# Kernel optimization log

Hardware: AMD Instinct MI355X
Metric: run time of the kernel (lower is better)

Reference implementation:

```python
import jax, jax.numpy as jnp
import numpy as np

DIM = 1024
HEAD_DIM = 64
NUM_HEADS = DIM // HEAD_DIM
SCALE = HEAD_DIM ** -0.5
B, N, M = 2, 1024, 2048


def setup_inputs() -> dict:
    key = jax.random.key(0)
    ks = jax.random.split(key, 7)
    x = jax.random.normal(ks[0], (B, N, DIM), dtype=jnp.float32)
    context = jax.random.normal(ks[1], (B, M, DIM), dtype=jnp.float32)
    # query row has at least one valid key (avoids all -inf softmax rows).
    mask = jax.random.bernoulli(ks[2], 0.9, (B, N, M))
    mask = mask.at[:, :, 0].set(True)
    # Linear params (torch nn.Linear convention: y = x @ W.T + b)
    sq = (1.0 / DIM) ** 0.5
    Wq = jax.random.uniform(ks[3], (DIM, DIM), minval=-sq, maxval=sq, dtype=jnp.float32)
    Wkv = jax.random.uniform(ks[4], (2 * DIM, DIM), minval=-sq, maxval=sq, dtype=jnp.float32)
    b_kv = jax.random.uniform(ks[5], (2 * DIM,), minval=-sq, maxval=sq, dtype=jnp.float32)
    Wo = jax.random.uniform(ks[6], (DIM, DIM), minval=-sq, maxval=sq, dtype=jnp.float32)
    return {"x": x, "context": context, "mask": mask,
            "Wq": Wq, "Wkv": Wkv, "b_kv": b_kv, "Wo": Wo}


def reference(x, context, mask, Wq, Wkv, b_kv, Wo):
    b, n, c = x.shape
    m = context.shape[1]
    h, d = NUM_HEADS, HEAD_DIM
    # Q projection (no bias): [b, n, h, d] -> bhnd
    q = (x @ Wq.T).reshape(b, n, h, d).transpose(0, 2, 1, 3)
    # KV projection (with bias): [b, m, 2, h, d]
    kv = (context @ Wkv.T + b_kv).reshape(b, m, 2, h, d)
    k = kv[:, :, 0].transpose(0, 2, 1, 3)  # bhmd
    v = kv[:, :, 1].transpose(0, 2, 1, 3)  # bhmd
    # scores: bhnm, scale applied after matmul as in the original
    attn = jnp.einsum('bhnd,bhmd->bhnm', q, k) * SCALE
    attn = jnp.where(mask[:, None, :, :], attn, -jnp.inf)
    attn = jax.nn.softmax(attn, axis=-1)
    out = jnp.einsum('bhnm,bhmd->bhnd', attn, v)
    out = out.transpose(0, 2, 1, 3).reshape(b, n, h * d)
    return out @ Wo.T
```

## Files before the change

kernel.cpp:

```cpp
#include <hip/hip_runtime.h>


typedef __attribute__((ext_vector_type(8))) short short8;
typedef __attribute__((ext_vector_type(4))) short short4v;
typedef __attribute__((ext_vector_type(4))) float f32x4;

#define SCL2E 0.18033688011112042592f

__device__ __forceinline__ float bf2f(short s) {
  unsigned u = ((unsigned)(unsigned short)s) << 16;
  return __uint_as_float(u);
}
__device__ __forceinline__ short f2bf(float f) {
  unsigned u = __float_as_uint(f);
  u += 0x7fffu + ((u >> 16) & 1u);
  return (short)(u >> 16);
}
__device__ __forceinline__ void gld_lds16(const void* gp, void* lp) {
  __builtin_amdgcn_global_load_lds(
      (const __attribute__((address_space(1))) unsigned int*)gp,
      (__attribute__((address_space(3))) unsigned int*)lp, 16, 0, 0);
}
__device__ __forceinline__ short4v cvt4(float4 v) {
  short4v o;
  o[0] = f2bf(v.x); o[1] = f2bf(v.y); o[2] = f2bf(v.z); o[3] = f2bf(v.w);
  return o;
}

__global__ __launch_bounds__(256) void prep(
    const unsigned char* __restrict__ mask, unsigned long long* __restrict__ pm,
    const float* __restrict__ Wq, const float* __restrict__ Wkv,
    const float* __restrict__ Wo, const float* __restrict__ x,
    const float* __restrict__ ctx, short* __restrict__ wqb,
    short* __restrict__ wkvb, short* __restrict__ wob,
    short* __restrict__ xb, short* __restrict__ ctxb) {
  const int row = blockIdx.x;
  const int wave = threadIdx.x >> 6, lane = threadIdx.x & 63;
  const unsigned char p8 = mask[lane * 4 + 1];
  const int p32 = ((const int*)mask)[lane * 2 + 1];
  const int shift =
      (__ballot(p8 != 0) != 0ull) ? 0 : ((__ballot(p32 != 0) != 0ull) ? 2 : 3);
  const size_t base = ((size_t)row * 2048) << shift;
#pragma unroll
  for (int j = 0; j < 8; j++) {
    const int c = wave * 512 + j * 64 + lane;
    const unsigned long long bits = __ballot(mask[base + ((size_t)c << shift)] != 0);
    if (lane == 0) pm[(size_t)row * 32 + wave * 8 + j] = bits;
  }
  const int gid = blockIdx.x * 256 + threadIdx.x;
  *(short4v*)(xb + (size_t)gid * 4) = cvt4(((const float4*)x)[gid]);
  *(short4v*)(ctxb + (size_t)gid * 4) = cvt4(((const float4*)ctx)[gid]);
  *(short4v*)(ctxb + (size_t)(gid + 524288) * 4) =
      cvt4(((const float4*)ctx)[gid + 524288]);
  *(short4v*)(wkvb + (size_t)gid * 4) = cvt4(((const float4*)Wkv)[gid]);
  if (gid < 262144) {
    *(short4v*)(wqb + (size_t)gid * 4) = cvt4(((const float4*)Wq)[gid]);
    *(short4v*)(wob + (size_t)gid * 4) = cvt4(((const float4*)Wo)[gid]);
  }
}

__global__ __launch_bounds__(256, 2)
void qkv_gemm(const short* __restrict__ xb, const short* __restrict__ ctxb,
              const short* __restrict__ wqb, const short* __restrict__ wkvb,
              const float* __restrict__ bias, short* __restrict__ qws,
              short* __restrict__ kws, short* __restrict__ vtws) {
  __shared__ __align__(16) short ldsA[8 * 512];
  __shared__ __align__(16) short ldsB[8 * 512];
  const int tid = threadIdx.x;
  const int wave = tid >> 6, lane = tid & 63;
  const int l15 = lane & 15, lg = lane >> 4;
  const int bx = blockIdx.x;
  const bool isKV = bx < 512;
  const int rows0 = isKV ? (bx >> 4) * 128 : ((bx - 512) >> 3) * 128;
  const int cols0 = isKV ? (bx & 15) * 128 : ((bx - 512) & 7) * 128;
  const short* Amat = isKV ? ctxb : xb;
  const short* Bw = isKV ? wkvb : wqb;
  const int wr = wave >> 1, wc = wave & 1;

  f32x4 acc[4][4];
#pragma unroll
  for (int i = 0; i < 4; i++)
#pragma unroll
    for (int j = 0; j < 4; j++) acc[i][j] = (f32x4){0.f, 0.f, 0.f, 0.f};

  const short* ga0 = Amat + (size_t)(rows0 + wave * 16 + l15) * 1024 + lg * 8;
  const short* ga1 = ga0 + (size_t)64 * 1024;
  const short* gb0 = Bw + (size_t)(cols0 + wave * 16 + l15) * 1024 + lg * 8;
  const short* gb1 = gb0 + (size_t)64 * 1024;
  short* la0 = &ldsA[wave * 512];
  short* la1 = &ldsA[(wave + 4) * 512];
  short* lb0 = &ldsB[wave * 512];
  short* lb1 = &ldsB[(wave + 4) * 512];

  for (int k0 = 0; k0 < 1024; k0 += 32) {
    __syncthreads();
    gld_lds16(ga0 + k0, la0);
    gld_lds16(ga1 + k0, la1);
    gld_lds16(gb0 + k0, lb0);
    gld_lds16(gb1 + k0, lb1);
    __syncthreads();
    short8 af[4], bfr[4];
#pragma unroll
    for (int t = 0; t < 4; t++)
      af[t] = *(const short8*)&ldsA[((wr * 4 + t) * 64 + lane) * 8];
#pragma unroll
    for (int t = 0; t < 4; t++)
      bfr[t] = *(const short8*)&ldsB[((wc * 4 + t) * 64 + lane) * 8];
#pragma unroll
    for (int i = 0; i < 4; i++)
#pragma unroll
      for (int j = 0; j < 4; j++)
        acc[i][j] =
            __builtin_amdgcn_mfma_f32_16x16x32_bf16(af[i], bfr[j], acc[i][j], 0, 0, 0);
  }

#pragma unroll
  for (int i = 0; i < 4; i++)
#pragma unroll
    for (int j = 0; j < 4; j++)
#pragma unroll
      for (int r = 0; r < 4; r++) {
        const int gr = rows0 + wr * 64 + i * 16 + lg * 4 + r;
        const int gc = cols0 + wc * 64 + j * 16 + l15;
        float v = acc[i][j][r];
        if (isKV) {
          v += bias[gc];
          const int b = gr >> 11, m = gr & 2047;
          const int kv = gc >> 10, hh = (gc >> 6) & 15, d = gc & 63;
          if (kv == 0)
            kws[((((size_t)b * 16 + hh) * 2048 + m) << 6) + d] = f2bf(v);
          else
            vtws[(((size_t)b * 16 + hh) * 64 + d) * 2048 + m] = f2bf(v);
        } else {
          const int b = gr >> 10, n = gr & 1023, hh = gc >> 6, d = gc & 63;
          qws[((((size_t)b * 16 + hh) * 1024 + n) << 6) + d] = f2bf(v * SCL2E);
        }
      }
}

__global__ __launch_bounds__(512, 2)
void attn_split(const short* __restrict__ Qg, const short* __restrict__ Kg,
                const short* __restrict__ Vtg,
                const unsigned int* __restrict__ pm,
                float* __restrict__ opart, float* __restrict__ lpart) {
  __shared__ __align__(16) short ldsK[8192];
  __shared__ __align__(16) short ldsV[8192];
  __shared__ __align__(16) short ldsP[17408];
  __shared__ __align__(16) short ones[512];
  const int tid = threadIdx.x;
  const int w = tid >> 6, lane = tid & 63;
  const int l15 = lane & 15, lg = lane >> 4;
  const int bx = blockIdx.x;
  const int bhid = bx & 31, qt = (bx >> 5) & 7, half = bx >> 8;
  const int b = bhid >> 4, h = bhid & 15;
  const int n0 = qt * 128, m_base = half * 1024;
  const size_t bh = (size_t)b * 16 + h;
  const short* Qb = Qg + (bh * 1024 + n0) * 64;
  const short* Kb = Kg + (bh << 17);
  const short* Vb = Vtg + (bh << 17);
  const unsigned int* pmw =
      pm + ((size_t)(b * 1024 + n0 + w * 16 + lg * 4) << 6) + (m_base >> 5);

  ones[tid] = 0x3F80;
#pragma unroll
  for (int ii = 0; ii < 2; ii++)
    gld_lds16(Qb + (size_t)(w * 16 + l15) * 64 + ii * 32 + lg * 8,
              &ldsP[(w * 2 + ii) * 512]);
  __syncthreads();
  short8 qf[2];
#pragma unroll
  for (int ks = 0; ks < 2; ks++)
    qf[ks] = *(const short8*)&ldsP[((w * 2 + ks) * 64 + lane) * 8];
  const short8 onesf = *(const short8*)&ones[lane * 8];

  f32x4 o[4], lacc;
#pragma unroll
  for (int ct = 0; ct < 4; ct++) o[ct] = (f32x4){0.f, 0.f, 0.f, 0.f};
  lacc = (f32x4){0.f, 0.f, 0.f, 0.f};
  short* Pme = &ldsP[w * 2176];

  uint4 mk[4], mkn[4];
#pragma unroll
  for (int r = 0; r < 4; r++) mk[r] = *(const uint4*)(pmw + (size_t)r * 64);

  for (int c = 0; c < 8; c++) {
    const int m0 = m_base + c * 128;
    __syncthreads();
#pragma unroll
    for (int ii = 0; ii < 2; ii++) {
      const int f = w * 2 + ii;
      const int t = f >> 1, ks = f & 1;
      gld_lds16(Kb + (size_t)(m0 + t * 16 + l15) * 64 + ks * 32 + lg * 8,
                &ldsK[f * 512]);
      const int ct = f >> 2, ks2 = f & 3;
      gld_lds16(Vb + (size_t)(ct * 16 + l15) * 2048 + (m0 + ks2 * 32 + lg * 8),
                &ldsV[f * 512]);
    }
    if (c < 7) {
#pragma unroll
      for (int r = 0; r < 4; r++)
        mkn[r] = *(const uint4*)(pmw + (size_t)r * 64 + (c + 1) * 4);
    }
    __syncthreads();

    f32x4 s[8];
#pragma unroll
    for (int t = 0; t < 8; t++) s[t] = (f32x4){0.f, 0.f, 0.f, 0.f};
#pragma unroll
    for (int t = 0; t < 8; t++)
#pragma unroll
      for (int ks = 0; ks < 2; ks++) {
        short8 kf = *(const short8*)&ldsK[((t * 2 + ks) * 64 + lane) * 8];
        s[t] = __builtin_amdgcn_mfma_f32_16x16x32_bf16(qf[ks], kf, s[t], 0, 0, 0);
      }

#pragma unroll
    for (int r = 0; r < 4; r++) {
      const unsigned int* mwp = (const unsigned int*)&mk[r];
#pragma unroll
      for (int t = 0; t < 8; t++) {
        const bool att = (mwp[t >> 1] >> (((t & 1) << 4) + l15)) & 1;
        const float p = exp2f(att ? s[t][r] : -1e30f);
        Pme[(lg * 4 + r) * 136 + t * 16 + l15] = f2bf(p);
      }
    }
    short8 pf[4];
#pragma unroll
    for (int ks2 = 0; ks2 < 4; ks2++)
      pf[ks2] = *(const short8*)&Pme[l15 * 136 + ks2 * 32 + lg * 8];
#pragma unroll
    for (int ct = 0; ct < 4; ct++)
#pragma unroll
      for (int ks2 = 0; ks2 < 4; ks2++) {
        short8 vf = *(const short8*)&ldsV[((ct * 4 + ks2) * 64 + lane) * 8];
        o[ct] = __builtin_amdgcn_mfma_f32_16x16x32_bf16(pf[ks2], vf, o[ct], 0, 0, 0);
      }
#pragma unroll
    for (int ks2 = 0; ks2 < 4; ks2++)
      lacc = __builtin_amdgcn_mfma_f32_16x16x32_bf16(pf[ks2], onesf, lacc, 0, 0, 0);
#pragma unroll
    for (int r = 0; r < 4; r++) mk[r] = mkn[r];
  }

#pragma unroll
  for (int ct = 0; ct < 4; ct++)
#pragma unroll
    for (int r = 0; r < 4; r++) {
      const int n = n0 + w * 16 + lg * 4 + r;
      opart[((size_t)half << 21) + (((size_t)b * 1024 + n) << 10) + h * 64 +
            ct * 16 + l15] = o[ct][r];
    }
  if (l15 == 0) {
#pragma unroll
    for (int r = 0; r < 4; r++) {
      const int n = n0 + w * 16 + lg * 4 + r;
      lpart[((size_t)half << 15) + bh * 1024 + n] = lacc[r];
    }
  }
}

__global__ __launch_bounds__(256) void combine(
    const float* __restrict__ opart, const float* __restrict__ lpart,
    short* __restrict__ ao) {
  const int gid = blockIdx.x * 256 + threadIdx.x;
  const size_t base = (size_t)gid * 4;
  const int row = (int)(base >> 10), col = (int)(base & 1023);
  const int b = row >> 10, n = row & 1023, h = col >> 6;
  const float4 o1 = *(const float4*)(opart + base);
  const float4 o2 = *(const float4*)(opart + (1u << 21) + base);
  const float l1 = lpart[(size_t)(b * 16 + h) * 1024 + n];
  const float l2 = lpart[(1u << 15) + (size_t)(b * 16 + h) * 1024 + n];
  const float inv = 1.f / fmaxf(l1 + l2, 1e-30f);
  short4v o;
  o[0] = f2bf((o1.x + o2.x) * inv); o[1] = f2bf((o1.y + o2.y) * inv);
  o[2] = f2bf((o1.z + o2.z) * inv); o[3] = f2bf((o1.w + o2.w) * inv);
  *(short4v*)(ao + base) = o;
}

__global__ __launch_bounds__(256, 2)
void o_gemm(const short* __restrict__ ao, const short* __restrict__ wob,
            float* __restrict__ Of) {
  __shared__ __align__(16) short ldsA[4 * 512];
  __shared__ __align__(16) short ldsB[4 * 512];
  const int tid = threadIdx.x;
  const int w = tid >> 6, lane = tid & 63;
  const int l15 = lane & 15, lg = lane >> 4;
  const int bx = blockIdx.x;
  const int rows0 = (bx >> 4) * 64, cols0 = (bx & 15) * 64;

  f32x4 acc[4];
#pragma unroll
  for (int j = 0; j < 4; j++) acc[j] = (f32x4){0.f, 0.f, 0.f, 0.f};

  const short* ga = ao + (size_t)(rows0 + w * 16 + l15) * 1024 + lg * 8;
  const short* gb = wob + (size_t)(cols0 + w * 16 + l15) * 1024 + lg * 8;
  short* la = &ldsA[w * 512];
  short* lb = &ldsB[w * 512];

  for (int k0 = 0; k0 < 1024; k0 += 32) {
    __syncthreads();
    gld_lds16(ga + k0, la);
    gld_lds16(gb + k0, lb);
    __syncthreads();
    const short8 af = *(const short8*)&ldsA[(w * 64 + lane) * 8];
#pragma unroll
    for (int j = 0; j < 4; j++) {
      const short8 bf = *(const short8*)&ldsB[(j * 64 + lane) * 8];
      acc[j] = __builtin_amdgcn_mfma_f32_16x16x32_bf16(af, bf, acc[j], 0, 0, 0);
    }
  }

#pragma unroll
  for (int j = 0; j < 4; j++)
#pragma unroll
    for (int r = 0; r < 4; r++) {
      const int gr = rows0 + w * 16 + lg * 4 + r;
      const int gc = cols0 + j * 16 + l15;
      Of[(size_t)gr * 1024 + gc] = acc[j][r];
    }
}

extern "C" void kernel_launch(void* const* d_in, const int* in_sizes, int n_in,
                              void* d_out, int out_size, void* d_ws, size_t ws_size,
                              hipStream_t stream) {
  const float* x   = (const float*)d_in[0];
  const float* ctx = (const float*)d_in[1];
  const unsigned char* mask = (const unsigned char*)d_in[2];
  const float* Wq  = (const float*)d_in[3];
  const float* Wkv = (const float*)d_in[4];
  const float* bkv = (const float*)d_in[5];
  const float* Wo  = (const float*)d_in[6];
  float* out = (float*)d_out;

  char* wsb = (char*)d_ws;
  short* qws  = (short*)(wsb);
  short* kws  = (short*)(wsb + (4u << 20));
  short* vtws = (short*)(wsb + (12u << 20));
  short* wqb  = (short*)(wsb + (20u << 20));
  short* wkvb = (short*)(wsb + (22u << 20));
  short* wob  = (short*)(wsb + (26u << 20));
  unsigned long long* pmws = (unsigned long long*)(wsb + (28u << 20));
  float* opart = (float*)(wsb + (29u << 20));
  float* lpart = (float*)(wsb + (45u << 20));
  short* xb   = (short*)(wsb + (29u << 20));
  short* ctxb = (short*)(wsb + (33u << 20));
  short* ao = (short*)(wsb + (20u << 20));

  prep<<<2048, 256, 0, stream>>>(mask, pmws, Wq, Wkv, Wo, x, ctx,
                                 wqb, wkvb, wob, xb, ctxb);
  qkv_gemm<<<640, 256, 0, stream>>>(xb, ctxb, wqb, wkvb, bkv, qws, kws, vtws);
  attn_split<<<512, 512, 0, stream>>>(qws, kws, vtws, (const unsigned int*)pmws,
                                      opart, lpart);
  combine<<<2048, 256, 0, stream>>>(opart, lpart, ao);
  o_gemm<<<512, 256, 0, stream>>>(ao, wob, out);
}
```

Before: 243.5 us.

## Double-buffer LDS tiles and widen K-step to 64 in projection GEMMs

Both the QKV and output-projection GEMMs now keep two LDS buffers. Each iteration issues the global-to-LDS loads for the next 64-wide K slice before running MFMAs on the current one. This removes one barrier per step and halves the number of loop iterations, so load latency can overlap with matrix math. In exchange the LDS footprint grows (64KB per block for the QKV GEMM), which could limit occupancy.

```diff
diff --git a/kernel.cpp b/kernel.cpp
--- a/kernel.cpp
+++ b/kernel.cpp
@@ -64,8 +64,8 @@
               const short* __restrict__ wqb, const short* __restrict__ wkvb,
               const float* __restrict__ bias, short* __restrict__ qws,
               short* __restrict__ kws, short* __restrict__ vtws) {
-  __shared__ __align__(16) short ldsA[8 * 512];
-  __shared__ __align__(16) short ldsB[8 * 512];
+  __shared__ __align__(16) short ldsA[2][16 * 512];
+  __shared__ __align__(16) short ldsB[2][16 * 512];
   const int tid = threadIdx.x;
   const int wave = tid >> 6, lane = tid & 63;
   const int l15 = lane & 15, lg = lane >> 4;
@@ -83,35 +83,43 @@
 #pragma unroll
     for (int j = 0; j < 4; j++) acc[i][j] = (f32x4){0.f, 0.f, 0.f, 0.f};
 
-  const short* ga0 = Amat + (size_t)(rows0 + wave * 16 + l15) * 1024 + lg * 8;
-  const short* ga1 = ga0 + (size_t)64 * 1024;
-  const short* gb0 = Bw + (size_t)(cols0 + wave * 16 + l15) * 1024 + lg * 8;
-  const short* gb1 = gb0 + (size_t)64 * 1024;
-  short* la0 = &ldsA[wave * 512];
-  short* la1 = &ldsA[(wave + 4) * 512];
-  short* lb0 = &ldsB[wave * 512];
-  short* lb1 = &ldsB[(wave + 4) * 512];
-
-  for (int k0 = 0; k0 < 1024; k0 += 32) {
+  const short* gaw0 = Amat + (size_t)(rows0 + wave * 16 + l15) * 1024 + lg * 8;
+  const short* gaw1 = gaw0 + (size_t)64 * 1024;
+  const short* gbw0 = Bw + (size_t)(cols0 + wave * 16 + l15) * 1024 + lg * 8;
+  const short* gbw1 = gbw0 + (size_t)64 * 1024;
+
+  auto stage = [&](int buf, int k0) {
+    gld_lds16(gaw0 + k0,      &ldsA[buf][(wave * 2 + 0) * 512]);
+    gld_lds16(gaw0 + k0 + 32, &ldsA[buf][(wave * 2 + 1) * 512]);
+    gld_lds16(gaw1 + k0,      &ldsA[buf][((wave + 4) * 2 + 0) * 512]);
+    gld_lds16(gaw1 + k0 + 32, &ldsA[buf][((wave + 4) * 2 + 1) * 512]);
+    gld_lds16(gbw0 + k0,      &ldsB[buf][(wave * 2 + 0) * 512]);
+    gld_lds16(gbw0 + k0 + 32, &ldsB[buf][(wave * 2 + 1) * 512]);
+    gld_lds16(gbw1 + k0,      &ldsB[buf][((wave + 4) * 2 + 0) * 512]);
+    gld_lds16(gbw1 + k0 + 32, &ldsB[buf][((wave + 4) * 2 + 1) * 512]);
+  };
+
+  stage(0, 0);
+  for (int it = 0; it < 16; ++it) {
+    const int buf = it & 1;
     __syncthreads();
-    gld_lds16(ga0 + k0, la0);
-    gld_lds16(ga1 + k0, la1);
-    gld_lds16(gb0 + k0, lb0);
-    gld_lds16(gb1 + k0, lb1);
-    __syncthreads();
-    short8 af[4], bfr[4];
-#pragma unroll
-    for (int t = 0; t < 4; t++)
-      af[t] = *(const short8*)&ldsA[((wr * 4 + t) * 64 + lane) * 8];
-#pragma unroll
-    for (int t = 0; t < 4; t++)
-      bfr[t] = *(const short8*)&ldsB[((wc * 4 + t) * 64 + lane) * 8];
-#pragma unroll
-    for (int i = 0; i < 4; i++)
-#pragma unroll
-      for (int j = 0; j < 4; j++)
-        acc[i][j] =
-            __builtin_amdgcn_mfma_f32_16x16x32_bf16(af[i], bfr[j], acc[i][j], 0, 0, 0);
+    if (it < 15) stage(buf ^ 1, (it + 1) * 64);
+#pragma unroll
+    for (int kb = 0; kb < 2; kb++) {
+      short8 af[4], bfr[4];
+#pragma unroll
+      for (int t = 0; t < 4; t++)
+        af[t] = *(const short8*)&ldsA[buf][((wr * 4 + t) * 2 + kb) * 512 + lane * 8];
+#pragma unroll
+      for (int t = 0; t < 4; t++)
+        bfr[t] = *(const short8*)&ldsB[buf][((wc * 4 + t) * 2 + kb) * 512 + lane * 8];
+#pragma unroll
+      for (int i = 0; i < 4; i++)
+#pragma unroll
+        for (int j = 0; j < 4; j++)
+          acc[i][j] =
+              __builtin_amdgcn_mfma_f32_16x16x32_bf16(af[i], bfr[j], acc[i][j], 0, 0, 0);
+    }
   }
 
 #pragma unroll
@@ -280,8 +288,8 @@
 __global__ __launch_bounds__(256, 2)
 void o_gemm(const short* __restrict__ ao, const short* __restrict__ wob,
             float* __restrict__ Of) {
-  __shared__ __align__(16) short ldsA[4 * 512];
-  __shared__ __align__(16) short ldsB[4 * 512];
+  __shared__ __align__(16) short ldsA[2][8 * 512];
+  __shared__ __align__(16) short ldsB[2][8 * 512];
   const int tid = threadIdx.x;
   const int w = tid >> 6, lane = tid & 63;
   const int l15 = lane & 15, lg = lane >> 4;
@@ -294,19 +302,27 @@
 
   const short* ga = ao + (size_t)(rows0 + w * 16 + l15) * 1024 + lg * 8;
   const short* gb = wob + (size_t)(cols0 + w * 16 + l15) * 1024 + lg * 8;
-  short* la = &ldsA[w * 512];
-  short* lb = &ldsB[w * 512];
-
-  for (int k0 = 0; k0 < 1024; k0 += 32) {
+
+  auto stage = [&](int buf, int k0) {
+    gld_lds16(ga + k0,      &ldsA[buf][(w * 2 + 0) * 512]);
+    gld_lds16(ga + k0 + 32, &ldsA[buf][(w * 2 + 1) * 512]);
+    gld_lds16(gb + k0,      &ldsB[buf][(w * 2 + 0) * 512]);
+    gld_lds16(gb + k0 + 32, &ldsB[buf][(w * 2 + 1) * 512]);
+  };
+
+  stage(0, 0);
+  for (int it = 0; it < 16; ++it) {
+    const int buf = it & 1;
     __syncthreads();
-    gld_lds16(ga + k0, la);
-    gld_lds16(gb + k0, lb);
-    __syncthreads();
-    const short8 af = *(const short8*)&ldsA[(w * 64 + lane) * 8];
-#pragma unroll
-    for (int j = 0; j < 4; j++) {
-      const short8 bf = *(const short8*)&ldsB[(j * 64 + lane) * 8];
-      acc[j] = __builtin_amdgcn_mfma_f32_16x16x32_bf16(af, bf, acc[j], 0, 0, 0);
+    if (it < 15) stage(buf ^ 1, (it + 1) * 64);
+#pragma unroll
+    for (int kb = 0; kb < 2; kb++) {
+      const short8 af = *(const short8*)&ldsA[buf][(w * 2 + kb) * 512 + lane * 8];
+#pragma unroll
+      for (int j = 0; j < 4; j++) {
+        const short8 bf = *(const short8*)&ldsB[buf][(j * 2 + kb) * 512 + lane * 8];
+        acc[j] = __builtin_amdgcn_mfma_f32_16x16x32_bf16(af, bf, acc[j], 0, 0, 0);
+      }
     }
   }
 
```

Measured after the change: 265.2 us. +8.9%, slower.

## Pre-tile GEMM operands so each k-step loads contiguous blocks into LDS

Applied to the files above, without the earlier changes.

The prep and combine kernels now write bf16 operands (x, context, weights, attention output) in a blocked tile layout that matches the MFMA fragment order of the later GEMMs. qkv_gemm and o_gemm then fetch each k-step tile as one contiguous 8KB/4KB chunk instead of 16-byte pieces strided by a 2KB row pitch. The aim is better coalescing and fewer DRAM pages and TLB entries touched by the global-to-LDS loads. In exchange, prep and combine do scattered 8-byte stores into the tiled layout, which may cost more than their old linear writes.

```diff
diff --git a/kernel.cpp b/kernel.cpp
--- a/kernel.cpp
+++ b/kernel.cpp
@@ -25,6 +25,14 @@
   short4v o;
   o[0] = f2bf(v.x); o[1] = f2bf(v.y); o[2] = f2bf(v.z); o[3] = f2bf(v.w);
   return o;
+}
+__device__ __forceinline__ size_t off128(int row, int k) {
+  return ((size_t)(((row >> 7) * 32 + (k >> 5)) * 8 + ((row >> 4) & 7)) << 9) +
+         (((((k >> 3) & 3) * 16 + (row & 15)) << 3) + (k & 7));
+}
+__device__ __forceinline__ size_t off64(int row, int k) {
+  return ((size_t)(((row >> 6) * 32 + (k >> 5)) * 4 + ((row >> 4) & 3)) << 9) +
+         (((((k >> 3) & 3) * 16 + (row & 15)) << 3) + (k & 7));
 }
 
 __global__ __launch_bounds__(256) void prep(
@@ -40,22 +48,32 @@
   const int p32 = ((const int*)mask)[lane * 2 + 1];
   const int shift =
       (__ballot(p8 != 0) != 0ull) ? 0 : ((__ballot(p32 != 0) != 0ull) ? 2 : 3);
-  const size_t base = ((size_t)row * 2048) << shift;
+  const size_t mbase = ((size_t)row * 2048) << shift;
 #pragma unroll
   for (int j = 0; j < 8; j++) {
     const int c = wave * 512 + j * 64 + lane;
-    const unsigned long long bits = __ballot(mask[base + ((size_t)c << shift)] != 0);
+    const unsigned long long bits = __ballot(mask[mbase + ((size_t)c << shift)] != 0);
     if (lane == 0) pm[(size_t)row * 32 + wave * 8 + j] = bits;
   }
   const int gid = blockIdx.x * 256 + threadIdx.x;
-  *(short4v*)(xb + (size_t)gid * 4) = cvt4(((const float4*)x)[gid]);
-  *(short4v*)(ctxb + (size_t)gid * 4) = cvt4(((const float4*)ctx)[gid]);
-  *(short4v*)(ctxb + (size_t)(gid + 524288) * 4) =
-      cvt4(((const float4*)ctx)[gid + 524288]);
-  *(short4v*)(wkvb + (size_t)gid * 4) = cvt4(((const float4*)Wkv)[gid]);
+  {
+    const int e = gid * 4, r = e >> 10, k = e & 1023;
+    *(short4v*)(xb + off128(r, k)) = cvt4(((const float4*)x)[gid]);
+  }
+  {
+    int e = gid * 4, r = e >> 10, k = e & 1023;
+    *(short4v*)(ctxb + off128(r, k)) = cvt4(((const float4*)ctx)[gid]);
+    e = (gid + 524288) * 4; r = e >> 10; k = e & 1023;
+    *(short4v*)(ctxb + off128(r, k)) = cvt4(((const float4*)ctx)[gid + 524288]);
+  }
+  {
+    const int e = gid * 4, r = e >> 10, k = e & 1023;
+    *(short4v*)(wkvb + off128(r, k)) = cvt4(((const float4*)Wkv)[gid]);
+  }
   if (gid < 262144) {
-    *(short4v*)(wqb + (size_t)gid * 4) = cvt4(((const float4*)Wq)[gid]);
-    *(short4v*)(wob + (size_t)gid * 4) = cvt4(((const float4*)Wo)[gid]);
+    const int e = gid * 4, r = e >> 10, k = e & 1023;
+    *(short4v*)(wqb + off128(r, k)) = cvt4(((const float4*)Wq)[gid]);
+    *(short4v*)(wob + off64(r, k)) = cvt4(((const float4*)Wo)[gid]);
   }
 }
 
@@ -71,8 +89,8 @@
   const int l15 = lane & 15, lg = lane >> 4;
   const int bx = blockIdx.x;
   const bool isKV = bx < 512;
-  const int rows0 = isKV ? (bx >> 4) * 128 : ((bx - 512) >> 3) * 128;
-  const int cols0 = isKV ? (bx & 15) * 128 : ((bx - 512) & 7) * 128;
+  const int rt = isKV ? (bx >> 4) : ((bx - 512) >> 3);
+  const int ct = isKV ? (bx & 15) : ((bx - 512) & 7);
   const short* Amat = isKV ? ctxb : xb;
   const short* Bw = isKV ? wkvb : wqb;
   const int wr = wave >> 1, wc = wave & 1;
@@ -83,21 +101,22 @@
 #pragma unroll
     for (int j = 0; j < 4; j++) acc[i][j] = (f32x4){0.f, 0.f, 0.f, 0.f};
 
-  const short* ga0 = Amat + (size_t)(rows0 + wave * 16 + l15) * 1024 + lg * 8;
-  const short* ga1 = ga0 + (size_t)64 * 1024;
-  const short* gb0 = Bw + (size_t)(cols0 + wave * 16 + l15) * 1024 + lg * 8;
-  const short* gb1 = gb0 + (size_t)64 * 1024;
+  const short* ga0 = Amat + (size_t)rt * 131072 + wave * 512 + lane * 8;
+  const short* ga1 = ga0 + 2048;
+  const short* gb0 = Bw + (size_t)ct * 131072 + wave * 512 + lane * 8;
+  const short* gb1 = gb0 + 2048;
   short* la0 = &ldsA[wave * 512];
   short* la1 = &ldsA[(wave + 4) * 512];
   short* lb0 = &ldsB[wave * 512];
   short* lb1 = &ldsB[(wave + 4) * 512];
 
   for (int k0 = 0; k0 < 1024; k0 += 32) {
-    __syncthreads();
-    gld_lds16(ga0 + k0, la0);
-    gld_lds16(ga1 + k0, la1);
-    gld_lds16(gb0 + k0, lb0);
-    gld_lds16(gb1 + k0, lb1);
+    const size_t koff = (size_t)(k0 >> 5) * 4096;
+    __syncthreads();
+    gld_lds16(ga0 + koff, la0);
+    gld_lds16(ga1 + koff, la1);
+    gld_lds16(gb0 + koff, lb0);
+    gld_lds16(gb1 + koff, lb1);
     __syncthreads();
     short8 af[4], bfr[4];
 #pragma unroll
@@ -120,8 +139,8 @@
     for (int j = 0; j < 4; j++)
 #pragma unroll
       for (int r = 0; r < 4; r++) {
-        const int gr = rows0 + wr * 64 + i * 16 + lg * 4 + r;
-        const int gc = cols0 + wc * 64 + j * 16 + l15;
+        const int gr = rt * 128 + wr * 64 + i * 16 + lg * 4 + r;
+        const int gc = ct * 128 + wc * 64 + j * 16 + l15;
         float v = acc[i][j][r];
         if (isKV) {
           v += bias[gc];
@@ -261,7 +280,7 @@
 
 __global__ __launch_bounds__(256) void combine(
     const float* __restrict__ opart, const float* __restrict__ lpart,
-    short* __restrict__ ao) {
+    short* __restrict__ aoT) {
   const int gid = blockIdx.x * 256 + threadIdx.x;
   const size_t base = (size_t)gid * 4;
   const int row = (int)(base >> 10), col = (int)(base & 1023);
@@ -274,11 +293,11 @@
   short4v o;
   o[0] = f2bf((o1.x + o2.x) * inv); o[1] = f2bf((o1.y + o2.y) * inv);
   o[2] = f2bf((o1.z + o2.z) * inv); o[3] = f2bf((o1.w + o2.w) * inv);
-  *(short4v*)(ao + base) = o;
+  *(short4v*)(aoT + off64(row, col)) = o;
 }
 
 __global__ __launch_bounds__(256, 2)
-void o_gemm(const short* __restrict__ ao, const short* __restrict__ wob,
+void o_gemm(const short* __restrict__ aoT, const short* __restrict__ wobT,
             float* __restrict__ Of) {
   __shared__ __align__(16) short ldsA[4 * 512];
   __shared__ __align__(16) short ldsB[4 * 512];
@@ -286,21 +305,22 @@
   const int w = tid >> 6, lane = tid & 63;
   const int l15 = lane & 15, lg = lane >> 4;
   const int bx = blockIdx.x;
-  const int rows0 = (bx >> 4) * 64, cols0 = (bx & 15) * 64;
+  const int rt = bx >> 4, ct = bx & 15;
 
   f32x4 acc[4];
 #pragma unroll
   for (int j = 0; j < 4; j++) acc[j] = (f32x4){0.f, 0.f, 0.f, 0.f};
 
-  const short* ga = ao + (size_t)(rows0 + w * 16 + l15) * 1024 + lg * 8;
-  const short* gb = wob + (size_t)(cols0 + w * 16 + l15) * 1024 + lg * 8;
+  const short* ga = aoT + (size_t)rt * 65536 + w * 512 + lane * 8;
+  const short* gb = wobT + (size_t)ct * 65536 + w * 512 + lane * 8;
   short* la = &ldsA[w * 512];
   short* lb = &ldsB[w * 512];
 
   for (int k0 = 0; k0 < 1024; k0 += 32) {
-    __syncthreads();
-    gld_lds16(ga + k0, la);
-    gld_lds16(gb + k0, lb);
+    const size_t koff = (size_t)(k0 >> 5) * 2048;
+    __syncthreads();
+    gld_lds16(ga + koff, la);
+    gld_lds16(gb + koff, lb);
     __syncthreads();
     const short8 af = *(const short8*)&ldsA[(w * 64 + lane) * 8];
 #pragma unroll
@@ -314,8 +334,8 @@
   for (int j = 0; j < 4; j++)
 #pragma unroll
     for (int r = 0; r < 4; r++) {
-      const int gr = rows0 + w * 16 + lg * 4 + r;
-      const int gc = cols0 + j * 16 + l15;
+      const int gr = rt * 64 + w * 16 + lg * 4 + r;
+      const int gc = ct * 64 + j * 16 + l15;
       Of[(size_t)gr * 1024 + gc] = acc[j][r];
     }
 }
```

After: 231.7 us. -4.9%, faster.
